# Performance work log

Hardware: AMD Instinct MI355X
Metric: run time of the kernel (lower is better)

## Reference

```python
import jax, jax.numpy as jnp
import numpy as np

REPR_OUT = (16, 16, 16)   # multiplicities for l=0,1,2
STRIDE = 2                # GatedBlock stride with smooth_stride=True -> low-pass+stride after gate
PAD = 2                   # conv padding
C_IN = 72                 # 8*1 + 8*3 + 8*5
C_OUT_GATED = 176         # 144 fields + 32 gate scalars
KSIZE = 5


def conv3d(x, w, stride, padding):
    return jax.lax.conv_general_dilated(
        x, w, window_strides=(stride,) * 3,
        padding=[(padding, padding)] * 3,
        dimension_numbers=('NCDHW', 'OIDHW', 'NCDHW'))


def low_pass_filter(z, scale, stride):
    # gaussian blur (sigma from scale) applied depthwise, then strided -- as in se3cnn
    sigma = 0.5 * (scale ** 2 - 1) ** 0.5
    size = int(1 + 2 * 2.5 * sigma)
    if size % 2 == 0:
        size += 1
    r = np.arange(size) - size // 2
    g1 = np.exp(-r.astype(np.float64) ** 2 / (2 * sigma ** 2))
    g = g1[:, None, None] * g1[None, :, None] * g1[None, None, :]
    g = (g / g.sum()).astype(np.float32)
    B, C = z.shape[0], z.shape[1]
    zz = z.reshape(B * C, 1, *z.shape[2:])
    out = conv3d(zz, jnp.asarray(g)[None, None], stride, size // 2)
    return out.reshape(B, C, *out.shape[2:])


def gate(y, scalar_bias, gate_bias):
    # y: [B, 176, X, Y, Z]; split into 144 field channels + 32 gate scalars
    size_out = sum(mul * (2 * n + 1) for n, mul in enumerate(REPR_OUT))
    B, _, nx, ny, nz = y.shape
    g = jax.nn.sigmoid(y[:, size_out:] + gate_bias[None, :, None, None, None])
    fields = []
    begin_y, begin_g = 0, 0
    for n, mul in enumerate(REPR_OUT):
        if mul == 0:
            continue
        dim = 2 * n + 1
        fy = y[:, begin_y:begin_y + mul * dim]
        if n == 0:
            # scalar fields: bias + relu (ScalarActivation)
            fields.append(jax.nn.relu(fy + scalar_bias[None, :, None, None, None]))
        else:
            fg = g[:, begin_g:begin_g + mul]
            begin_g += mul
            f = fy.reshape(B, mul, dim, nx, ny, nz) * fg[:, :, None]  # broadcast gate over 2l+1
            fields.append(f.reshape(B, mul * dim, nx, ny, nz))
        begin_y += mul * dim
    return jnp.concatenate(fields, axis=1)  # [B, 144, X, Y, Z]


def setup_inputs() -> dict:
    key = jax.random.key(0)
    k1, k2, k3, k4 = jax.random.split(key, 4)
    fan_in = C_IN * KSIZE ** 3
    x = jax.random.normal(k1, (4, C_IN, 32, 32, 32), dtype=jnp.float32)
    W = jax.random.normal(k2, (C_OUT_GATED, C_IN, KSIZE, KSIZE, KSIZE), dtype=jnp.float32) / np.sqrt(fan_in)
    scalar_bias = jax.random.normal(k3, (REPR_OUT[0],), dtype=jnp.float32) * 0.1
    gate_bias = jax.random.normal(k4, (sum(REPR_OUT[1:]),), dtype=jnp.float32) * 0.1
    return {'x': x, 'W': W, 'scalar_bias': scalar_bias, 'gate_bias': gate_bias}


def reference(x, W, scalar_bias, gate_bias):
    y = conv3d(x, W, 1, PAD)                 # SE3 conv at stride 1 (smooth_stride)
    z = gate(y, scalar_bias, gate_bias)      # per-irrep gated nonlinearity
    z = low_pass_filter(z, STRIDE, STRIDE)   # gaussian low-pass + stride 2
    return z
```

## Files before the change

kernel.cpp:

```cpp
#include <hip/hip_runtime.h>
#include <cstdint>
#include <cstddef>

typedef short short8 __attribute__((ext_vector_type(8)));
typedef float floatx4 __attribute__((ext_vector_type(4)));
typedef unsigned short u16;

__device__ __forceinline__ u16 f2bf(float f) {
    unsigned u = __float_as_uint(f);
    u += 0x7FFFu + ((u >> 16) & 1u);
    return (u16)(u >> 16);
}
__device__ __forceinline__ float bf2f(u16 h) {
    return __uint_as_float(((unsigned)h) << 16);
}

__device__ __forceinline__ void gload_lds16(const u16* g, u16* l) {
    __builtin_amdgcn_global_load_lds(
        (const __attribute__((address_space(1))) void*)g,
        (__attribute__((address_space(3))) void*)l, 16, 0, 0);
}

__global__ __launch_bounds__(256) void k_transpose_x(const float* __restrict__ x,
                                                     u16* __restrict__ xt) {
    __shared__ float tile[72 * 33];
    const int bx = blockIdx.x;
    const int tid = threadIdx.x;
    const int b = bx >> 10, d = (bx >> 5) & 31, h = bx & 31;
    const float* src = x + (size_t)b * 72 * 32768 + d * 1024 + h * 32;
    for (int e = tid; e < 2304; e += 256) {
        int ci = e >> 5, w = e & 31;
        tile[ci * 33 + w] = src[(size_t)ci * 32768 + w];
    }
    __syncthreads();
    u16* dst = xt + (size_t)bx * 2304;
    for (int e = tid; e < 2304; e += 256) {
        int w = e / 72, ci = e - w * 72;
        dst[e] = f2bf(tile[ci * 33 + w]);
    }
}

__global__ __launch_bounds__(256) void k_prep_w(const float* __restrict__ W,
                                                u16* __restrict__ wt) {
    const int gid = blockIdx.x * 256 + threadIdx.x;
    const int frag = gid >> 6, lane = gid & 63;
    const int nb = frag % 11;
    int t = frag / 11;
    const int kb = t % 12;
    t = t / 12;
    const int kh = t % 5, kd = t / 5;
    const int n = lane & 15, q8 = (lane >> 4) * 8;
    const int co = nb * 16 + n;
    u16 v[8] __attribute__((aligned(16)));
    #pragma unroll
    for (int j = 0; j < 8; ++j) {
        int k = kb * 32 + q8 + j;
        u16 r = 0;
        if (k < 360) {
            int kw = k / 72, ci = k - kw * 72;
            r = f2bf(W[((size_t)co * 72 + ci) * 125 + kd * 25 + kh * 5 + kw]);
        }
        v[j] = r;
    }
    *(uint4*)(wt + (size_t)gid * 8) = *(const uint4*)v;
}

#define LP 2592
#define MFMA_BF16 __builtin_amdgcn_mfma_f32_16x16x32_bf16

template<int CB>
__device__ __forceinline__ void conv_body(const u16* __restrict__ xt,
                                          const u16* __restrict__ wt,
                                          const float* __restrict__ scalar_bias,
                                          const float* __restrict__ gate_bias,
                                          u16* __restrict__ zt,
                                          u16* sx, u16* sB,
                                          int b, int d, int h0,
                                          int tid, int lane, int wv,
                                          int c15, int q) {
    constexpr int NF = CB ? 6 : 5;

    floatx4 acc[4][NF];
    #pragma unroll
    for (int i = 0; i < 4; ++i) {
        #pragma unroll
        for (int j = 0; j < NF; ++j) acc[i][j] = (floatx4){0.f, 0.f, 0.f, 0.f};
    }

    const int laneA = c15 * 72 + q * 8;

    for (int kd = 0; kd < 5; ++kd) {
        const int dp = d + kd - 2;
        if (dp < 0 || dp >= 32) continue;
        const u16* wt_kd = wt + (size_t)kd * 5 * 67584;

        const u16* srcbase = xt + (size_t)((b * 32 + dp) * 32) * 2304;
        for (int idx = tid; idx < 12 * 324; idx += 256) {
            int r = idx / 324, c = idx - r * 324;
            int hp = h0 + r - 2;
            uint4 val = make_uint4(0u, 0u, 0u, 0u);
            if (hp >= 0 && hp < 32 && c >= 18 && c < 306)
                val = *(const uint4*)(srcbase + (size_t)hp * 2304 + (c * 8 - 144));
            *(uint4*)(&sx[r * LP + c * 8]) = val;
        }

        auto stage = [&](int kk, int s) {
            #pragma unroll
            for (int t = 0; t < 2; ++t) {
                const int f = wv + t * 4;
                if (f < NF) {
                    const int nb = CB ? ((f == 5) ? 10 : (f + 4))
                                      : ((f == 4) ? 9 : f);
                    gload_lds16(wt_kd + (size_t)kk * 5632 + nb * 512 + lane * 8,
                                sB + s * 3072 + f * 512);
                }
            }
        };

        stage(0, 0);
        stage(1, 1);
        __syncthreads();

        int kh = 0, kb = 0, s0 = 0;
        #pragma unroll 1
        for (int kk = 0; kk < 60; ++kk) {
            int s2 = s0 + 2; if (s2 >= 3) s2 -= 3;
            if (kk < 58) stage(kk + 2, s2);
            const u16* ap = sx + (2 * wv + kh) * LP + laneA + kb * 32;
            short8 A0 = *(const short8*)(ap);
            short8 A1 = *(const short8*)(ap + 1152);
            short8 A2 = *(const short8*)(ap + LP);
            short8 A3 = *(const short8*)(ap + LP + 1152);
            const u16* bb = sB + s0 * 3072 + lane * 8;
            __builtin_amdgcn_s_setprio(1);
            #pragma unroll
            for (int f = 0; f < NF; ++f) {
                short8 bv = *(const short8*)(bb + f * 512);
                acc[0][f] = MFMA_BF16(A0, bv, acc[0][f], 0, 0, 0);
                acc[1][f] = MFMA_BF16(A1, bv, acc[1][f], 0, 0, 0);
                acc[2][f] = MFMA_BF16(A2, bv, acc[2][f], 0, 0, 0);
                acc[3][f] = MFMA_BF16(A3, bv, acc[3][f], 0, 0, 0);
            }
            __builtin_amdgcn_s_setprio(0);
            __syncthreads();
            if (++kb == 12) { kb = 0; ++kh; }
            if (++s0 == 3) s0 = 0;
        }
    }

    constexpr int GF = NF - 1;
    constexpr int NGATED = CB ? 5 : 3;
    int   slA[NGATED];
    float gbA[NGATED];
    #pragma unroll
    for (int j = 0; j < NGATED; ++j) {
        const int nb = CB ? (j + 4) : (j + 1);
        const int idx = (nb - 1) * 16 + c15;
        const int mul = (nb <= 3) ? (idx / 3) : (16 + (idx - 48) / 5);
        slA[j] = (lane & 48) | (mul & 15);
        gbA[j] = gate_bias[mul];
    }
    const float sb = CB ? 0.f : scalar_bias[c15];
    #pragma unroll
    for (int mi = 0; mi < 4; ++mi) {
        const int hl = 2 * wv + (mi >> 1);
        const int wh = mi & 1;
        const size_t zrow0 = (size_t)((b * 32 + d) * 32 + (h0 + hl)) * 32;
        #pragma unroll
        for (int r = 0; r < 4; ++r) {
            const int w = wh * 16 + q * 4 + r;
            u16* zp = zt + (zrow0 + w) * 144;
            const float gv = acc[mi][GF][r];
            if (CB == 0)
                zp[c15] = f2bf(fmaxf(acc[mi][0][r] + sb, 0.f));
            #pragma unroll
            for (int j = 0; j < NGATED; ++j) {
                const int nb = CB ? (j + 4) : (j + 1);
                float ys = __shfl(gv, slA[j], 64);
                float g  = 1.f / (1.f + __expf(-(ys + gbA[j])));
                zp[nb * 16 + c15] = f2bf(acc[mi][CB ? j : (j + 1)][r] * g);
            }
        }
    }
}

__global__ __launch_bounds__(256, 2) void k_conv(const u16* __restrict__ xt,
                                                 const u16* __restrict__ wt,
                                                 const float* __restrict__ scalar_bias,
                                                 const float* __restrict__ gate_bias,
                                                 u16* __restrict__ zt) {
    __shared__ __align__(16) u16 sx[12 * LP];
    __shared__ __align__(16) u16 sB[3 * 3072];
    const int bx = blockIdx.x;
    const int swz = (bx & 7) * 128 + (bx >> 3);
    const int cb = swz & 1, ht = (swz >> 1) & 3, d = (swz >> 3) & 31, b = swz >> 8;
    const int h0 = ht * 8;
    const int tid = threadIdx.x, lane = tid & 63, wv = tid >> 6;
    const int c15 = lane & 15, q = lane >> 4;

    if (cb == 0)
        conv_body<0>(xt, wt, scalar_bias, gate_bias, zt, sx, sB, b, d, h0, tid, lane, wv, c15, q);
    else
        conv_body<1>(xt, wt, scalar_bias, gate_bias, zt, sx, sB, b, d, h0, tid, lane, wv, c15, q);
}

__global__ __launch_bounds__(256) void k_lowpass(const u16* __restrict__ zt,
                                                 float* __restrict__ out) {
    const int gid = blockIdx.x * 256 + threadIdx.x;
    const int row = gid / 288;
    const int it  = gid - row * 288;
    const int c8 = it >> 4, ow = it & 15;
    const int oh = row & 15, od = (row >> 4) & 15, b = row >> 8;
    const float lw[5] = {0.03208210f, 0.23705644f, 0.46172277f, 0.23705644f, 0.03208210f};
    float a[8];
    #pragma unroll
    for (int j = 0; j < 8; ++j) a[j] = 0.f;
    for (int kd = 0; kd < 5; ++kd) {
        const int dz = 2 * od + kd - 2;
        if (dz < 0 || dz >= 32) continue;
        for (int kh = 0; kh < 5; ++kh) {
            const int hz = 2 * oh + kh - 2;
            if (hz < 0 || hz >= 32) continue;
            const float whd = lw[kd] * lw[kh];
            const u16* base = zt + (size_t)((b * 32 + dz) * 32 + hz) * 32 * 144 + c8 * 8;
            #pragma unroll
            for (int kw = 0; kw < 5; ++kw) {
                const int wz = 2 * ow + kw - 2;
                if (wz < 0 || wz >= 32) continue;
                const float wt3 = whd * lw[kw];
                u16 v[8] __attribute__((aligned(16)));
                *(uint4*)v = *(const uint4*)(base + (size_t)wz * 144);
                #pragma unroll
                for (int j = 0; j < 8; ++j) a[j] += wt3 * bf2f(v[j]);
            }
        }
    }
    const int c0 = c8 * 8;
    float* op = out + ((size_t)b * 144 + c0) * 4096 + od * 256 + oh * 16 + ow;
    #pragma unroll
    for (int j = 0; j < 8; ++j) op[(size_t)j * 4096] = a[j];
}

extern "C" void kernel_launch(void* const* d_in, const int* in_sizes, int n_in,
                              void* d_out, int out_size, void* d_ws, size_t ws_size,
                              hipStream_t stream) {
    const float* x  = (const float*)d_in[0];
    const float* W  = (const float*)d_in[1];
    const float* sb = (const float*)d_in[2];
    const float* gb = (const float*)d_in[3];
    float* out = (float*)d_out;

    char* ws = (char*)d_ws;
    u16* xt = (u16*)(ws);
    u16* wt = (u16*)(ws + 18874368);
    u16* zt = (u16*)(ws + 22253568);

    hipLaunchKernelGGL(k_transpose_x, dim3(4096), dim3(256), 0, stream, x, xt);
    hipLaunchKernelGGL(k_prep_w,      dim3(825),  dim3(256), 0, stream, W, wt);
    hipLaunchKernelGGL(k_conv,        dim3(1024), dim3(256), 0, stream, xt, wt, sb, gb, zt);
    hipLaunchKernelGGL(k_lowpass,     dim3(1152), dim3(256), 0, stream, zt, out);
}
```

Measured before the change: 570.9 us.

## Register double-buffer B fragments, pad LDS rows, and split lowpass into separable passes

The conv main loop is unrolled by six with B fragments prefetched into registers one step ahead, the LDS slot size shrinks to NF*512, and the activation row pitch is padded to change LDS bank mapping. The gaussian low-pass is split into a D/H pass writing an fp32 intermediate into the workspace (reusing the xt region) and a separate W pass, which cuts the taps per output. This trades an extra kernel launch and an intermediate round-trip through memory for fewer loads per output and better overlap of LDS reads with MFMA.

```diff
diff --git a/kernel.cpp b/kernel.cpp
--- a/kernel.cpp
+++ b/kernel.cpp
@@ -65,7 +65,7 @@
     *(uint4*)(wt + (size_t)gid * 8) = *(const uint4*)v;
 }
 
-#define LP 2592
+#define LP 2624
 #define MFMA_BF16 __builtin_amdgcn_mfma_f32_16x16x32_bf16
 
 template<int CB>
@@ -79,6 +79,7 @@
                                           int tid, int lane, int wv,
                                           int c15, int q) {
     constexpr int NF = CB ? 6 : 5;
+    constexpr int SLOT = NF * 512;
 
     floatx4 acc[4][NF];
     #pragma unroll
@@ -88,15 +89,24 @@
     }
 
     const int laneA = c15 * 72 + q * 8;
+    const u16* sxA = sx + 2 * wv * LP + laneA;
+    short8 Bc[NF], Bn[NF];
+
+    auto stage = [&](int kk_, int s_) {
+        const u16* gs_ = wt + (size_t)kk_ * 5632 + lane * 8;
+        (void)gs_;
+    };
+    (void)stage;
 
     for (int kd = 0; kd < 5; ++kd) {
         const int dp = d + kd - 2;
         if (dp < 0 || dp >= 32) continue;
         const u16* wt_kd = wt + (size_t)kd * 5 * 67584;
 
+        __syncthreads();
         const u16* srcbase = xt + (size_t)((b * 32 + dp) * 32) * 2304;
-        for (int idx = tid; idx < 12 * 324; idx += 256) {
-            int r = idx / 324, c = idx - r * 324;
+        for (int idx = tid; idx < 12 * 328; idx += 256) {
+            int r = idx / 328, c = idx - r * 328;
             int hp = h0 + r - 2;
             uint4 val = make_uint4(0u, 0u, 0u, 0u);
             if (hp >= 0 && hp < 32 && c >= 18 && c < 306)
@@ -104,48 +114,68 @@
             *(uint4*)(&sx[r * LP + c * 8]) = val;
         }
 
-        auto stage = [&](int kk, int s) {
+        #define STAGE_SLOT(kk_, s_) do {                                            \
+            const u16* gs_ = wt_kd + (size_t)(kk_) * 5632 + lane * 8;               \
+            u16* ds_ = sB + (s_) * SLOT;                                            \
+            {   const int nb0_ = CB ? (wv + 4) : ((wv == 4) ? 9 : wv);              \
+                gload_lds16(gs_ + nb0_ * 512, ds_ + wv * 512); }                    \
+            if (wv + 4 < NF) {                                                      \
+                const int nb1_ = CB ? 10 : 9;    \
+                const int f1_  = wv + 4;                                            \
+                const int nbx_ = CB ? ((f1_ == 5) ? 10 : (f1_ + 4))                 \
+                                    : ((f1_ == 4) ? 9 : f1_);                       \
+                (void)nb1_;                                                         \
+                gload_lds16(gs_ + nbx_ * 512, ds_ + f1_ * 512);                     \
+            }                                                                       \
+        } while (0)
+
+        STAGE_SLOT(0, 0);
+        STAGE_SLOT(1, 1);
+        __syncthreads();
+
+        {
+            const u16* bp = sB + 0 * SLOT + lane * 8;
             #pragma unroll
-            for (int t = 0; t < 2; ++t) {
-                const int f = wv + t * 4;
-                if (f < NF) {
-                    const int nb = CB ? ((f == 5) ? 10 : (f + 4))
-                                      : ((f == 4) ? 9 : f);
-                    gload_lds16(wt_kd + (size_t)kk * 5632 + nb * 512 + lane * 8,
-                                sB + s * 3072 + f * 512);
-                }
-            }
-        };
-
-        stage(0, 0);
-        stage(1, 1);
-        __syncthreads();
-
-        int kh = 0, kb = 0, s0 = 0;
+            for (int f = 0; f < NF; ++f) Bc[f] = *(const short8*)(bp + f * 512);
+        }
+
+        int aoff = 0, kb = 0;
+        #define STEP(CUR, NXT, kkc_, pslot_, sslot_) do {                           \
+            const u16* ap_ = sxA + aoff;                                            \
+            short8 A0_ = *(const short8*)(ap_);                                     \
+            short8 A1_ = *(const short8*)(ap_ + 1152);                              \
+            short8 A2_ = *(const short8*)(ap_ + LP);                                \
+            short8 A3_ = *(const short8*)(ap_ + LP + 1152);                         \
+            const u16* bp_ = sB + (pslot_) * SLOT + lane * 8;                       \
+            _Pragma("unroll")                                                       \
+            for (int f = 0; f < NF; ++f) NXT[f] = *(const short8*)(bp_ + f * 512);  \
+            if ((kkc_) + 2 < 60) STAGE_SLOT((kkc_) + 2, (sslot_));                  \
+            __builtin_amdgcn_s_setprio(1);                                          \
+            _Pragma("unroll")                                                       \
+            for (int f = 0; f < NF; ++f) {                                          \
+                acc[0][f] = MFMA_BF16(A0_, CUR[f], acc[0][f], 0, 0, 0);             \
+                acc[1][f] = MFMA_BF16(A1_, CUR[f], acc[1][f], 0, 0, 0);             \
+                acc[2][f] = MFMA_BF16(A2_, CUR[f], acc[2][f], 0, 0, 0);             \
+                acc[3][f] = MFMA_BF16(A3_, CUR[f], acc[3][f], 0, 0, 0);             \
+            }                                                                       \
+            __builtin_amdgcn_s_setprio(0);                                          \
+            __syncthreads();                                                        \
+            aoff += 32;                                                             \
+            if (++kb == 12) { kb = 0; aoff += LP - 384; }                           \
+        } while (0)
+
         #pragma unroll 1
-        for (int kk = 0; kk < 60; ++kk) {
-            int s2 = s0 + 2; if (s2 >= 3) s2 -= 3;
-            if (kk < 58) stage(kk + 2, s2);
-            const u16* ap = sx + (2 * wv + kh) * LP + laneA + kb * 32;
-            short8 A0 = *(const short8*)(ap);
-            short8 A1 = *(const short8*)(ap + 1152);
-            short8 A2 = *(const short8*)(ap + LP);
-            short8 A3 = *(const short8*)(ap + LP + 1152);
-            const u16* bb = sB + s0 * 3072 + lane * 8;
-            __builtin_amdgcn_s_setprio(1);
-            #pragma unroll
-            for (int f = 0; f < NF; ++f) {
-                short8 bv = *(const short8*)(bb + f * 512);
-                acc[0][f] = MFMA_BF16(A0, bv, acc[0][f], 0, 0, 0);
-                acc[1][f] = MFMA_BF16(A1, bv, acc[1][f], 0, 0, 0);
-                acc[2][f] = MFMA_BF16(A2, bv, acc[2][f], 0, 0, 0);
-                acc[3][f] = MFMA_BF16(A3, bv, acc[3][f], 0, 0, 0);
-            }
-            __builtin_amdgcn_s_setprio(0);
-            __syncthreads();
-            if (++kb == 12) { kb = 0; ++kh; }
-            if (++s0 == 3) s0 = 0;
-        }
+        for (int m = 0; m < 10; ++m) {
+            const int kk0 = m * 6;
+            STEP(Bc, Bn, kk0 + 0, 1, 2);
+            STEP(Bn, Bc, kk0 + 1, 2, 0);
+            STEP(Bc, Bn, kk0 + 2, 0, 1);
+            STEP(Bn, Bc, kk0 + 3, 1, 2);
+            STEP(Bc, Bn, kk0 + 4, 2, 0);
+            STEP(Bn, Bc, kk0 + 5, 0, 1);
+        }
+        #undef STEP
+        #undef STAGE_SLOT
     }
 
     constexpr int GF = NF - 1;
@@ -190,7 +220,7 @@
                                                  const float* __restrict__ gate_bias,
                                                  u16* __restrict__ zt) {
     __shared__ __align__(16) u16 sx[12 * LP];
-    __shared__ __align__(16) u16 sB[3 * 3072];
+    __shared__ __align__(16) u16 sB[3 * 6 * 512];
     const int bx = blockIdx.x;
     const int swz = (bx & 7) * 128 + (bx >> 3);
     const int cb = swz & 1, ht = (swz >> 1) & 3, d = (swz >> 3) & 31, b = swz >> 8;
@@ -204,13 +234,15 @@
         conv_body<1>(xt, wt, scalar_bias, gate_bias, zt, sx, sB, b, d, h0, tid, lane, wv, c15, q);
 }
 
-__global__ __launch_bounds__(256) void k_lowpass(const u16* __restrict__ zt,
-                                                 float* __restrict__ out) {
+__global__ __launch_bounds__(256) void k_lowpass_dh(const u16* __restrict__ zt,
+                                                    float* __restrict__ tmp) {
     const int gid = blockIdx.x * 256 + threadIdx.x;
-    const int row = gid / 288;
-    const int it  = gid - row * 288;
-    const int c8 = it >> 4, ow = it & 15;
-    const int oh = row & 15, od = (row >> 4) & 15, b = row >> 8;
+    const int c8 = gid % 18;
+    int r = gid / 18;
+    const int w  = r & 31; r >>= 5;
+    const int oh = r & 15; r >>= 4;
+    const int od = r & 15; r >>= 4;
+    const int b  = r;
     const float lw[5] = {0.03208210f, 0.23705644f, 0.46172277f, 0.23705644f, 0.03208210f};
     float a[8];
     #pragma unroll
@@ -221,19 +253,43 @@
         for (int kh = 0; kh < 5; ++kh) {
             const int hz = 2 * oh + kh - 2;
             if (hz < 0 || hz >= 32) continue;
-            const float whd = lw[kd] * lw[kh];
-            const u16* base = zt + (size_t)((b * 32 + dz) * 32 + hz) * 32 * 144 + c8 * 8;
+            const float wt2 = lw[kd] * lw[kh];
+            const u16* p = zt + ((size_t)((b * 32 + dz) * 32 + hz) * 32 + w) * 144 + c8 * 8;
+            u16 v[8] __attribute__((aligned(16)));
+            *(uint4*)v = *(const uint4*)p;
             #pragma unroll
-            for (int kw = 0; kw < 5; ++kw) {
-                const int wz = 2 * ow + kw - 2;
-                if (wz < 0 || wz >= 32) continue;
-                const float wt3 = whd * lw[kw];
-                u16 v[8] __attribute__((aligned(16)));
-                *(uint4*)v = *(const uint4*)(base + (size_t)wz * 144);
-                #pragma unroll
-                for (int j = 0; j < 8; ++j) a[j] += wt3 * bf2f(v[j]);
-            }
-        }
+            for (int j = 0; j < 8; ++j) a[j] += wt2 * bf2f(v[j]);
+        }
+    }
+    float* tp = tmp + ((size_t)(((b * 16 + od) * 16 + oh) * 32) + w) * 144 + c8 * 8;
+    *(float4*)(tp)     = make_float4(a[0], a[1], a[2], a[3]);
+    *(float4*)(tp + 4) = make_float4(a[4], a[5], a[6], a[7]);
+}
+
+__global__ __launch_bounds__(256) void k_lowpass_w(const float* __restrict__ tmp,
+                                                   float* __restrict__ out) {
+    const int gid = blockIdx.x * 256 + threadIdx.x;
+    const int c8 = gid % 18;
+    int r = gid / 18;
+    const int ow = r & 15; r >>= 4;
+    const int oh = r & 15; r >>= 4;
+    const int od = r & 15; r >>= 4;
+    const int b  = r;
+    const float lw[5] = {0.03208210f, 0.23705644f, 0.46172277f, 0.23705644f, 0.03208210f};
+    float a[8];
+    #pragma unroll
+    for (int j = 0; j < 8; ++j) a[j] = 0.f;
+    const float* tb = tmp + ((size_t)(((b * 16 + od) * 16 + oh) * 32)) * 144 + c8 * 8;
+    #pragma unroll
+    for (int kw = 0; kw < 5; ++kw) {
+        const int wz = 2 * ow + kw - 2;
+        if (wz < 0 || wz >= 32) continue;
+        const float wt1 = lw[kw];
+        const float* p = tb + (size_t)wz * 144;
+        float4 v0 = *(const float4*)(p);
+        float4 v1 = *(const float4*)(p + 4);
+        a[0] += wt1 * v0.x; a[1] += wt1 * v0.y; a[2] += wt1 * v0.z; a[3] += wt1 * v0.w;
+        a[4] += wt1 * v1.x; a[5] += wt1 * v1.y; a[6] += wt1 * v1.z; a[7] += wt1 * v1.w;
     }
     const int c0 = c8 * 8;
     float* op = out + ((size_t)b * 144 + c0) * 4096 + od * 256 + oh * 16 + ow;
@@ -254,9 +310,11 @@
     u16* xt = (u16*)(ws);
     u16* wt = (u16*)(ws + 18874368);
     u16* zt = (u16*)(ws + 22253568);
+    float* tmp = (float*)(ws);
 
     hipLaunchKernelGGL(k_transpose_x, dim3(4096), dim3(256), 0, stream, x, xt);
     hipLaunchKernelGGL(k_prep_w,      dim3(825),  dim3(256), 0, stream, W, wt);
     hipLaunchKernelGGL(k_conv,        dim3(1024), dim3(256), 0, stream, xt, wt, sb, gb, zt);
-    hipLaunchKernelGGL(k_lowpass,     dim3(1152), dim3(256), 0, stream, zt, out);
-}
+    hipLaunchKernelGGL(k_lowpass_dh,  dim3(2304), dim3(256), 0, stream, zt, tmp);
+    hipLaunchKernelGGL(k_lowpass_w,   dim3(1152), dim3(256), 0, stream, tmp, out);
+}
```

Result: faster. 497.4 us (-12.9%).
